# Kernel optimization log

Hardware: AMD Instinct MI355X
Metric: run time of the kernel (lower is better)

The kernel has to match this reference:

```python
import jax, jax.numpy as jnp
import numpy as np

B, W, M = 16, 32, 512
NH, HALF, K, H = 64, 32, 8, 8
LK = W // 2               # long-conv kernel size
LOUT = W - 2 * (LK - 1)   # = 2 (dilated valid conv output length)
NSP = 10                  # n_spatial (hardcoded in module)
GC1_IN = (1 + LOUT) * K   # 24


def setup_inputs() -> dict:
    key = jax.random.key(0)
    ks = jax.random.split(key, 23)
    def n(k, shp, s=0.1):
        return jax.random.normal(k, shp, jnp.float32) * s
    return dict(
        x=jax.random.normal(ks[0], (B, W, M), jnp.float32),
        adj=jax.random.uniform(ks[1], (M, M), jnp.float32) / M,  # row-normalized-ish dense adj
        Wih=n(ks[2], (NH, 1)), Whh=n(ks[3], (NH, NH)),
        bih=n(ks[4], (NH,)), bhh=n(ks[5], (NH,)),
        W1=n(ks[6], (HALF, NH)), W2=n(ks[7], (HALF, NH)), b1=n(ks[8], (HALF,)),
        V=n(ks[9], (HALF,)), bv=n(ks[10], (1,)),
        Wb=n(ks[11], (M, M)), wb=n(ks[12], (1,)),
        conv_w=n(ks[13], (K, 1, W)), conv_b=n(ks[14], (K,)),
        convl_w=n(ks[15], (K, 1, LK)), convl_b=n(ks[16], (K,)),
        gc1_w=n(ks[17], (GC1_IN, NH)), gc1_b=n(ks[18], (NH,)),
        gc2_w=n(ks[19], (NH, NSP)), gc2_b=n(ks[20], (NSP,)),
        out_w=n(ks[21], (H, NSP + NH)), out_b=n(ks[22], (H,)),
    )


def reference(x, adj, Wih, Whh, bih, bhh, W1, W2, b1, V, bv, Wb, wb,
              conv_w, conv_b, convl_w, convl_b, gc1_w, gc1_b, gc2_w, gc2_b,
              out_w, out_b):
    b = x.shape[0]
    # [b, w, m] -> per-node sequences [b*m, w]
    seq = jnp.transpose(x, (0, 2, 1)).reshape(b * M, W)

    # vanilla tanh RNN, input_size=1 (batched over all b*m series)
    inp = seq[:, :, None] * Wih[:, 0] + (bih + bhh)          # [b*m, w, nh]
    def step(h, it):
        return jnp.tanh(it + h @ Whh.T), None
    h0 = jnp.zeros((b * M, NH), x.dtype)
    last_hid, _ = jax.lax.scan(step, h0, jnp.swapaxes(inp, 0, 1))
    last_hid = last_hid.reshape(b, M, NH)                    # out_temporal

    # pairwise additive attention: a[b,i,j] = V . elu(W1 h_j + W2 h_i + b1) + bv
    e1 = last_hid @ W1.T                                     # [b, m, half] (j role)
    e2 = last_hid @ W2.T                                     # [b, m, half] (i role)
    a = jax.nn.elu(e2[:, :, None, :] + e1[:, None, :, :] + b1)  # [b,m,m,half]
    a_mx = a @ V + bv                                        # [b, m, m]
    # F.normalize(p=2, dim=1)
    norm = jnp.sqrt(jnp.sum(a_mx * a_mx, axis=1, keepdims=True))
    a_mx = a_mx / jnp.maximum(norm, 1e-12)

    # per-node short conv (kernel == window -> out len 1) as a single matmul
    r_short = seq @ conv_w[:, 0, :].T + conv_b               # [b*m, k]
    # per-node dilated long conv, batched over all b*m series
    r_long = jax.lax.conv_general_dilated(
        seq[:, None, :], convl_w, window_strides=(1,), padding='VALID',
        rhs_dilation=(2,), dimension_numbers=('NCW', 'OIW', 'NCW'))
    r_long = r_long + convl_b[None, :, None]                 # [b*m, k, LOUT]
    r = jnp.concatenate([r_short[:, :, None], r_long], axis=-1)  # [b*m, k, 1+LOUT]
    r = jax.nn.relu(r.reshape(b, M, GC1_IN))

    # gated mix of static normalized adj and learned attention adj
    c = jax.nn.sigmoid(a_mx @ Wb + wb)
    adj_mix = adj[None] * c + a_mx * (1.0 - c)               # [b, m, m]

    # two dense graph conv layers: relu(adj @ (h @ W) + b)
    h1 = jax.nn.relu(adj_mix @ (r @ gc1_w) + gc1_b)          # [b, m, nh]
    out_spatial = jax.nn.relu(adj_mix @ (h1 @ gc2_w) + gc2_b)  # [b, m, nsp]

    feat = jnp.concatenate([out_spatial, last_hid], axis=-1)  # [b, m, nsp+nh]
    out = feat @ out_w.T + out_b                              # [b, m, h]
    return jnp.transpose(out, (0, 2, 1))                      # [b, h, m]
```

## Files before the change

### kernel.cpp

```cpp
#include <hip/hip_runtime.h>


typedef __attribute__((ext_vector_type(8))) short bf16x8;
typedef __attribute__((ext_vector_type(4))) float f32x4;
#define MFMA16 __builtin_amdgcn_mfma_f32_16x16x32_bf16

__device__ __forceinline__ unsigned short f2bf(float f) {
    unsigned u = __float_as_uint(f);
    u += 0x7fff + ((u >> 16) & 1);
    return (unsigned short)(u >> 16);
}
__device__ __forceinline__ float bf2f(unsigned short h) {
    return __uint_as_float(((unsigned)h) << 16);
}
__device__ __forceinline__ float fast_tanh(float x) {
    float e = __expf(2.f * x);
    return 1.f - 2.f / (e + 1.f);
}

__global__ __launch_bounds__(256) void fused1_kernel(
    const float* __restrict__ x, const float* __restrict__ Wih,
    const float* __restrict__ Whh, const float* __restrict__ bih,
    const float* __restrict__ bhh, const float* __restrict__ W1,
    const float* __restrict__ W2, float* __restrict__ lh,
    float* __restrict__ e1, float* __restrict__ e2,
    const float* __restrict__ conv_w, const float* __restrict__ conv_b,
    const float* __restrict__ convl_w, const float* __restrict__ convl_b,
    const float* __restrict__ gc1_w, unsigned short* __restrict__ rgT,
    const float* __restrict__ Wb, unsigned short* __restrict__ WbT,
    float* __restrict__ nrmss)
{
    __shared__ __align__(16) char smem[12160];
    int blk = blockIdx.x, t = threadIdx.x;

    if (blk < 256) {
        int wid = t >> 6, lane = t & 63;
        int rowblk = blk * 32;
        int b = rowblk >> 9, mb = rowblk & 511;
        float* xs = (float*)smem;
        unsigned short* hs = (unsigned short*)(smem + 4096);
        float* rrs = (float*)(smem + 8704);

        for (int u = t; u < 1024; u += 256) {
            int tt = u >> 5, c = u & 31;
            xs[tt * 32 + c] = x[(b * 32 + tt) * 512 + mb + c];
        }
        for (int u = t; u < 2304; u += 256) hs[u] = 0;
        __syncthreads();

        if (wid < 2) {
            int l15 = lane & 15, quad = lane >> 4;
            int row0 = rowblk + wid * 16;
            unsigned short* hw0 = hs + wid * 1152;

            bf16x8 afr[4][2];
#pragma unroll
            for (int mt = 0; mt < 4; ++mt)
#pragma unroll
                for (int hf = 0; hf < 2; ++hf) {
                    const float* src = Whh + (16 * mt + l15) * 64 + 32 * hf + quad * 8;
                    union { bf16x8 v; unsigned short u[8]; } tmp;
#pragma unroll
                    for (int j = 0; j < 8; ++j) tmp.u[j] = f2bf(src[j]);
                    afr[mt][hf] = tmp.v;
                }
            bf16x8 wfr[2][2][2];
#pragma unroll
            for (int e = 0; e < 2; ++e)
#pragma unroll
                for (int nt = 0; nt < 2; ++nt)
#pragma unroll
                    for (int kf = 0; kf < 2; ++kf) {
                        const float* Wsrc = (e ? W2 : W1);
                        const float* src = Wsrc + (16 * nt + l15) * 64 + 32 * kf + quad * 8;
                        union { bf16x8 v; unsigned short u[8]; } tmp;
#pragma unroll
                        for (int j = 0; j < 8; ++j) tmp.u[j] = f2bf(src[j]);
                        wfr[e][nt][kf] = tmp.v;
                    }
            float wihv[4][4], bsv[4][4];
#pragma unroll
            for (int mt = 0; mt < 4; ++mt)
#pragma unroll
                for (int r = 0; r < 4; ++r) {
                    int n = 16 * mt + quad * 4 + r;
                    wihv[mt][r] = Wih[n];
                    bsv[mt][r]  = bih[n] + bhh[n];
                }

            float th[4][4];
            for (int tstep = 0; tstep < 32; ++tstep) {
                bf16x8 b0 = *(bf16x8*)(hw0 + l15 * 72 + quad * 8);
                bf16x8 b1 = *(bf16x8*)(hw0 + l15 * 72 + 32 + quad * 8);
                float xt = xs[tstep * 32 + wid * 16 + l15];
                f32x4 acc[4];
#pragma unroll
                for (int mt = 0; mt < 4; ++mt) {
                    f32x4 z = {0.f, 0.f, 0.f, 0.f};
                    acc[mt] = MFMA16(afr[mt][0], b0, z, 0, 0, 0);
                    acc[mt] = MFMA16(afr[mt][1], b1, acc[mt], 0, 0, 0);
                }
#pragma unroll
                for (int mt = 0; mt < 4; ++mt) {
                    ushort4 hwv;
#pragma unroll
                    for (int r = 0; r < 4; ++r)
                        th[mt][r] = fast_tanh(acc[mt][r] + xt * wihv[mt][r] + bsv[mt][r]);
                    hwv.x = f2bf(th[mt][0]); hwv.y = f2bf(th[mt][1]);
                    hwv.z = f2bf(th[mt][2]); hwv.w = f2bf(th[mt][3]);
                    *(ushort4*)(hw0 + l15 * 72 + 16 * mt + quad * 4) = hwv;
                }
            }
#pragma unroll
            for (int mt = 0; mt < 4; ++mt)
                *(float4*)(lh + (row0 + l15) * 64 + 16 * mt + quad * 4) =
                    make_float4(th[mt][0], th[mt][1], th[mt][2], th[mt][3]);

            bf16x8 a0 = *(bf16x8*)(hw0 + l15 * 72 + quad * 8);
            bf16x8 a1 = *(bf16x8*)(hw0 + l15 * 72 + 32 + quad * 8);
#pragma unroll
            for (int e = 0; e < 2; ++e) {
                float* dst = e ? e2 : e1;
#pragma unroll
                for (int nt = 0; nt < 2; ++nt) {
                    f32x4 z = {0.f, 0.f, 0.f, 0.f};
                    f32x4 ee = MFMA16(a0, wfr[e][nt][0], z, 0, 0, 0);
                    ee = MFMA16(a1, wfr[e][nt][1], ee, 0, 0, 0);
#pragma unroll
                    for (int r = 0; r < 4; ++r)
                        dst[(row0 + quad * 4 + r) * 32 + 16 * nt + l15] = ee[r];
                }
            }
        } else {
            int wid2 = wid - 2;
#pragma unroll
            for (int rep = 0; rep < 2; ++rep) {
                int task = rep * 64 + lane;
                int rl = wid2 * 16 + (task >> 3);
                int k  = task & 7;
                float s = conv_b[k];
                for (int w = 0; w < 32; ++w) s += xs[w * 32 + rl] * conv_w[k * 32 + w];
                float l0 = convl_b[k], l1 = l0;
                for (int tt = 0; tt < 16; ++tt) {
                    float wv = convl_w[k * 16 + tt];
                    l0 += xs[(2 * tt) * 32 + rl] * wv;
                    l1 += xs[(2 * tt + 1) * 32 + rl] * wv;
                }
                rrs[rl * 25 + k * 3 + 0] = fmaxf(s, 0.f);
                rrs[rl * 25 + k * 3 + 1] = fmaxf(l0, 0.f);
                rrs[rl * 25 + k * 3 + 2] = fmaxf(l1, 0.f);
            }
            __builtin_amdgcn_wave_barrier();
            int rl = wid2 * 16 + (lane & 15);
            int nb = lane >> 4;
#pragma unroll
            for (int q = 0; q < 16; ++q) {
                int n = nb * 16 + q;
                float acc = 0.f;
#pragma unroll
                for (int c = 0; c < 24; ++c) acc += rrs[rl * 25 + c] * gc1_w[c * 64 + n];
                rgT[b * 32768 + n * 512 + mb + rl] = f2bf(acc);
            }
        }
    } else if (blk < 512) {
        int bid = blk - 256;
        int nb = (bid & 15) * 32, kb = (bid >> 4) * 32;
        float* tile = (float*)smem;
        for (int u = t; u < 1024; u += 256) {
            int r = u >> 5, c = u & 31;
            tile[r * 33 + c] = Wb[(kb + r) * 512 + nb + c];
        }
        __syncthreads();
        for (int u = t; u < 1024; u += 256) {
            int r = u >> 5, c = u & 31;
            WbT[(nb + r) * 512 + kb + c] = f2bf(tile[c * 33 + r]);
        }
    } else {
        nrmss[(blk - 512) * 256 + t] = 0.f;
    }
}

__global__ __launch_bounds__(256) void amx_kernel(
    const float* __restrict__ e1, const float* __restrict__ e2,
    const float* __restrict__ b1p, const float* __restrict__ Vp,
    const float* __restrict__ bvp, unsigned short* __restrict__ amxb,
    float* __restrict__ nrmss)
{
    int bb = blockIdx.z;
    int i0 = blockIdx.y * 64, j0 = blockIdx.x * 64;
    __shared__ float e2s[64][33], e1s[64][33];
    __shared__ float Vs[32];
    __shared__ float red[16][68];
    int t = threadIdx.x;
    for (int u = t; u < 2048; u += 256) {
        int r = u >> 5, c = u & 31;
        e2s[r][c] = e2[(bb * 512 + i0 + r) * 32 + c];
        e1s[r][c] = e1[(bb * 512 + j0 + r) * 32 + c] + b1p[c];
    }
    if (t < 32) Vs[t] = Vp[t];
    __syncthreads();
    int ti = (t >> 4) * 4, tj = (t & 15) * 4;
    float acc[4][4] = {};
#pragma unroll
    for (int h = 0; h < 32; ++h) {
        float vv = Vs[h];
        float xi[4], yj[4], Exi[4], Eyj[4];
#pragma unroll
        for (int p = 0; p < 4; ++p) { xi[p] = e2s[ti + p][h]; Exi[p] = __expf(xi[p]); }
#pragma unroll
        for (int q = 0; q < 4; ++q) { yj[q] = e1s[tj + q][h]; Eyj[q] = __expf(yj[q]); }
#pragma unroll
        for (int p = 0; p < 4; ++p)
#pragma unroll
            for (int q = 0; q < 4; ++q) {
                float v = xi[p] + yj[q];
                float prod = Exi[p] * Eyj[q];
                float el = v > 0.f ? v : prod - 1.f;
                acc[p][q] += vv * el;
            }
    }
    float bv = bvp[0];
    float ss[4] = {0.f, 0.f, 0.f, 0.f};
#pragma unroll
    for (int p = 0; p < 4; ++p) {
        float v0 = acc[p][0] + bv, v1 = acc[p][1] + bv;
        float v2 = acc[p][2] + bv, v3 = acc[p][3] + bv;
        ushort4 o;
        o.x = f2bf(v0); o.y = f2bf(v1); o.z = f2bf(v2); o.w = f2bf(v3);
        *(ushort4*)(amxb + (bb * 512 + i0 + ti + p) * 512 + j0 + tj) = o;
        ss[0] += v0 * v0; ss[1] += v1 * v1; ss[2] += v2 * v2; ss[3] += v3 * v3;
    }
#pragma unroll
    for (int q = 0; q < 4; ++q) red[t >> 4][tj + q] = ss[q];
    __syncthreads();
    if (t < 64) {
        float s = 0.f;
#pragma unroll
        for (int g = 0; g < 16; ++g) s += red[g][t];
        atomicAdd(&nrmss[bb * 512 + j0 + t], s);
    }
}

__global__ __launch_bounds__(256) void gemm_adjmix(
    const unsigned short* __restrict__ amxb, const unsigned short* __restrict__ WbT,
    const float* __restrict__ wbp, const float* __restrict__ adj,
    const float* __restrict__ nrmss, unsigned short* __restrict__ adjmix)
{
    int bb = blockIdx.z;
    int i0 = blockIdx.y * 64, j0 = blockIdx.x * 64;
    __shared__ __align__(16) short As[64 * 72];
    __shared__ __align__(16) short Bs[64 * 72];
    __shared__ float rn[512];
    int t = threadIdx.x, w = t >> 6, lane = t & 63;
    int l15 = lane & 15, quad = lane >> 4;
    for (int u = t; u < 512; u += 256)
        rn[u] = 1.f / fmaxf(sqrtf(nrmss[bb * 512 + u]), 1e-12f);
    const unsigned short* Ag = amxb + bb * 262144;
    f32x4 acc[4] = {};
    for (int kk = 1; kk <= 8; ++kk) {
        int k0 = (j0 + 64 * kk) & 511;
        __syncthreads();
#pragma unroll
        for (int u0 = 0; u0 < 2; ++u0) {
            int u = t + u0 * 256;
            int i = u >> 3, o = u & 7;
            *(int4*)(Bs + i * 72 + o * 8) =
                *(const int4*)(WbT + (j0 + i) * 512 + k0 + o * 8);
            union { int4 v; unsigned short us[8]; } ur;
            ur.v = *(const int4*)(Ag + (i0 + i) * 512 + k0 + o * 8);
            union { int4 v; unsigned short us[8]; } ow;
#pragma unroll
            for (int c = 0; c < 8; ++c)
                ow.us[c] = f2bf(bf2f(ur.us[c]) * rn[k0 + o * 8 + c]);
            *(int4*)(As + i * 72 + o * 8) = ow.v;
        }
        __syncthreads();
        bf16x8 a0 = *(bf16x8*)(As + (16 * w + l15) * 72 + quad * 8);
        bf16x8 a1 = *(bf16x8*)(As + (16 * w + l15) * 72 + 32 + quad * 8);
#pragma unroll
        for (int nt = 0; nt < 4; ++nt) {
            bf16x8 b0 = *(bf16x8*)(Bs + (16 * nt + l15) * 72 + quad * 8);
            bf16x8 b1 = *(bf16x8*)(Bs + (16 * nt + l15) * 72 + 32 + quad * 8);
            acc[nt] = MFMA16(a0, b0, acc[nt], 0, 0, 0);
            acc[nt] = MFMA16(a1, b1, acc[nt], 0, 0, 0);
        }
    }
    float wb = wbp[0];
#pragma unroll
    for (int nt = 0; nt < 4; ++nt)
#pragma unroll
    for (int r = 0; r < 4; ++r) {
        int il = 16 * w + quad * 4 + r;
        int jl = 16 * nt + l15;
        int i = i0 + il, j = j0 + jl;
        float s  = acc[nt][r] + wb;
        float cv = 1.f / (1.f + __expf(-s));
        float am = bf2f((unsigned short)As[il * 72 + jl]);
        float ad = adj[i * 512 + j];
        adjmix[(bb * 512 + i) * 512 + j] = f2bf(ad * cv + am * (1.f - cv));
    }
}

__global__ __launch_bounds__(256) void gemm_h1(
    const unsigned short* __restrict__ adjmix, const unsigned short* __restrict__ rgT,
    const float* __restrict__ gc1_b, const float* __restrict__ gc2_w,
    float* __restrict__ h1g)
{
    int bb = blockIdx.y;
    int i0 = blockIdx.x * 32;
    __shared__ __align__(16) short As[32 * 72];
    __shared__ __align__(16) short Bs[64 * 72];
    __shared__ float h1s[32][72];
    int t = threadIdx.x, w = t >> 6, lane = t & 63;
    int l15 = lane & 15, quad = lane >> 4;
    int rt = w & 1, ntb = (w >> 1) * 2;
    const unsigned short* Ag = adjmix + bb * 262144;
    const unsigned short* Bg = rgT + bb * 32768;
    f32x4 acc[2] = {};
    for (int k0 = 0; k0 < 512; k0 += 64) {
        __syncthreads();
        {
            int i = t >> 3, o = t & 7;
            *(int4*)(As + i * 72 + o * 8) =
                *(const int4*)(Ag + (i0 + i) * 512 + k0 + o * 8);
        }
#pragma unroll
        for (int u0 = 0; u0 < 2; ++u0) {
            int u = t + u0 * 256;
            int i = u >> 3, o = u & 7;
            *(int4*)(Bs + i * 72 + o * 8) =
                *(const int4*)(Bg + i * 512 + k0 + o * 8);
        }
        __syncthreads();
        bf16x8 a0 = *(bf16x8*)(As + (16 * rt + l15) * 72 + quad * 8);
        bf16x8 a1 = *(bf16x8*)(As + (16 * rt + l15) * 72 + 32 + quad * 8);
#pragma unroll
        for (int q = 0; q < 2; ++q) {
            int nt = ntb + q;
            bf16x8 b0 = *(bf16x8*)(Bs + (16 * nt + l15) * 72 + quad * 8);
            bf16x8 b1 = *(bf16x8*)(Bs + (16 * nt + l15) * 72 + 32 + quad * 8);
            acc[q] = MFMA16(a0, b0, acc[q], 0, 0, 0);
            acc[q] = MFMA16(a1, b1, acc[q], 0, 0, 0);
        }
    }
#pragma unroll
    for (int q = 0; q < 2; ++q)
#pragma unroll
    for (int r = 0; r < 4; ++r) {
        int il = 16 * rt + quad * 4 + r;
        int j = 16 * (ntb + q) + l15;
        h1s[il][j] = fmaxf(acc[q][r] + gc1_b[j], 0.f);
    }
    __syncthreads();
    for (int u = t; u < 320; u += 256) {
        int row = u / 10, ns = u - row * 10;
        float a2 = 0.f;
#pragma unroll
        for (int j = 0; j < 64; ++j) a2 += h1s[row][j] * gc2_w[j * 10 + ns];
        h1g[(bb * 512 + i0 + row) * 10 + ns] = a2;
    }
}

__global__ __launch_bounds__(256) void ospout_kernel(
    const unsigned short* __restrict__ adjmix, const float* __restrict__ h1g,
    const float* __restrict__ gc2_b, const float* __restrict__ lh,
    const float* __restrict__ out_w, const float* __restrict__ out_b,
    float* __restrict__ out)
{
    int r0 = blockIdx.x * 16;
    int bb = r0 >> 9;
    int wid = threadIdx.x >> 6, lane = threadIdx.x & 63;
    __shared__ float Bsm[10][512];
    __shared__ float ow[8][80];
    __shared__ float ob[8], g2b[10];
    for (int u = threadIdx.x; u < 5120; u += 256) {
        int k = u / 10, ns = u - k * 10;
        Bsm[ns][k] = h1g[bb * 5120 + u];
    }
    if (threadIdx.x < 8)  ob[threadIdx.x]  = out_b[threadIdx.x];
    if (threadIdx.x < 10) g2b[threadIdx.x] = gc2_b[threadIdx.x];
    for (int u = threadIdx.x; u < 592; u += 256) {
        int hh = u / 74, c = u - hh * 74;
        ow[hh][c] = out_w[u];
    }
    __syncthreads();
#pragma unroll
    for (int half = 0; half < 4; ++half) {
        int row = r0 + half * 4 + wid, m = row & 511;
        const unsigned short* Ar = adjmix + row * 512;
        float a[8];
#pragma unroll
        for (int q = 0; q < 8; ++q) a[q] = bf2f(Ar[lane + 64 * q]);
        float os[10];
#pragma unroll
        for (int ns = 0; ns < 10; ++ns) {
            float s = 0.f;
#pragma unroll
            for (int q = 0; q < 8; ++q) s += a[q] * Bsm[ns][lane + 64 * q];
#pragma unroll
            for (int off = 32; off; off >>= 1) s += __shfl_xor(s, off);
            os[ns] = fmaxf(s + g2b[ns], 0.f);
        }
        float lv = lh[row * 64 + lane];
#pragma unroll
        for (int hh = 0; hh < 8; ++hh) {
            float t1 = lv * ow[hh][10 + lane];
#pragma unroll
            for (int off = 32; off; off >>= 1) t1 += __shfl_xor(t1, off);
            if (lane == hh) {
                float acc = ob[hh] + t1;
#pragma unroll
                for (int ns = 0; ns < 10; ++ns) acc += os[ns] * ow[hh][ns];
                out[bb * 4096 + hh * 512 + m] = acc;
            }
        }
    }
}

extern "C" void kernel_launch(void* const* d_in, const int* in_sizes, int n_in,
                              void* d_out, int out_size, void* d_ws, size_t ws_size,
                              hipStream_t stream)
{
    const float* x       = (const float*)d_in[0];
    const float* adj     = (const float*)d_in[1];
    const float* Wih     = (const float*)d_in[2];
    const float* Whh     = (const float*)d_in[3];
    const float* bih     = (const float*)d_in[4];
    const float* bhh     = (const float*)d_in[5];
    const float* W1      = (const float*)d_in[6];
    const float* W2      = (const float*)d_in[7];
    const float* b1      = (const float*)d_in[8];
    const float* V       = (const float*)d_in[9];
    const float* bv      = (const float*)d_in[10];
    const float* Wb      = (const float*)d_in[11];
    const float* wb      = (const float*)d_in[12];
    const float* conv_w  = (const float*)d_in[13];
    const float* conv_b  = (const float*)d_in[14];
    const float* convl_w = (const float*)d_in[15];
    const float* convl_b = (const float*)d_in[16];
    const float* gc1_w   = (const float*)d_in[17];
    const float* gc1_b   = (const float*)d_in[18];
    const float* gc2_w   = (const float*)d_in[19];
    const float* gc2_b   = (const float*)d_in[20];
    const float* out_w   = (const float*)d_in[21];
    const float* out_b   = (const float*)d_in[22];

    float* ws    = (float*)d_ws;
    float* lh    = ws;
    float* e1    = lh + 524288;
    float* e2    = e1 + 262144;
    float* nrmss = e2 + 262144;
    float* h1g   = nrmss + 8192;
    unsigned short* amxb    = (unsigned short*)(h1g + 81920);
    unsigned short* adjmixb = amxb + 4194304;
    unsigned short* WbT     = adjmixb + 4194304;
    unsigned short* rgT     = WbT + 262144;

    fused1_kernel<<<544, 256, 0, stream>>>(
        x, Wih, Whh, bih, bhh, W1, W2, lh, e1, e2,
        conv_w, conv_b, convl_w, convl_b, gc1_w, rgT, Wb, WbT, nrmss);
    amx_kernel<<<dim3(8, 8, 16), 256, 0, stream>>>(e1, e2, b1, V, bv,
                                                   amxb, nrmss);
    gemm_adjmix<<<dim3(8, 8, 16), 256, 0, stream>>>(amxb, WbT, wb, adj,
                                                    nrmss, adjmixb);
    gemm_h1<<<dim3(16, 16), 256, 0, stream>>>(adjmixb, rgT, gc1_b, gc2_w, h1g);
    ospout_kernel<<<512, 256, 0, stream>>>(adjmixb, h1g, gc2_b, lh,
                                           out_w, out_b, (float*)d_out);
}
```

Before: 208.0 us.

## Fuse five kernels into one persistent kernel with global atomic barriers

Merges the RNN/conv, attention, adjmix GEMM, h1 GEMM and output kernels into a single 512-block persistent kernel. The stages are separated by a software grid barrier built on an atomic counter that is reset with a memset before launch. This removes four kernel launch gaps and their tail effects. The cost is spin-wait barrier overhead, and the kernel deadlocks unless all 512 blocks are co-resident, which it relies on launch_bounds(256,2) to allow.

```diff
diff --git a/kernel.cpp b/kernel.cpp
--- a/kernel.cpp
+++ b/kernel.cpp
@@ -4,6 +4,8 @@
 typedef __attribute__((ext_vector_type(8))) short bf16x8;
 typedef __attribute__((ext_vector_type(4))) float f32x4;
 #define MFMA16 __builtin_amdgcn_mfma_f32_16x16x32_bf16
+
+#define NBLK 512u
 
 __device__ __forceinline__ unsigned short f2bf(float f) {
     unsigned u = __float_as_uint(f);
@@ -18,20 +20,40 @@
     return 1.f - 2.f / (e + 1.f);
 }
 
-__global__ __launch_bounds__(256) void fused1_kernel(
-    const float* __restrict__ x, const float* __restrict__ Wih,
-    const float* __restrict__ Whh, const float* __restrict__ bih,
-    const float* __restrict__ bhh, const float* __restrict__ W1,
-    const float* __restrict__ W2, float* __restrict__ lh,
+__device__ __forceinline__ void gbar(unsigned* cnt, unsigned target) {
+    __threadfence();
+    __syncthreads();
+    if (threadIdx.x == 0) {
+        __hip_atomic_fetch_add(cnt, 1u, __ATOMIC_ACQ_REL, __HIP_MEMORY_SCOPE_AGENT);
+        while (__hip_atomic_load(cnt, __ATOMIC_ACQUIRE, __HIP_MEMORY_SCOPE_AGENT) < target)
+            __builtin_amdgcn_s_sleep(2);
+    }
+    __syncthreads();
+    __threadfence();
+}
+
+__global__ __launch_bounds__(256, 2) void cola_fused(
+    const float* __restrict__ x, const float* __restrict__ adj,
+    const float* __restrict__ Wih, const float* __restrict__ Whh,
+    const float* __restrict__ bih, const float* __restrict__ bhh,
+    const float* __restrict__ W1, const float* __restrict__ W2,
+    const float* __restrict__ b1p, const float* __restrict__ Vp,
+    const float* __restrict__ bvp, const float* __restrict__ Wb,
+    const float* __restrict__ wbp, const float* __restrict__ conv_w,
+    const float* __restrict__ conv_b, const float* __restrict__ convl_w,
+    const float* __restrict__ convl_b, const float* __restrict__ gc1_w,
+    const float* __restrict__ gc1_b, const float* __restrict__ gc2_w,
+    const float* __restrict__ gc2_b, const float* __restrict__ out_w,
+    const float* __restrict__ out_b, float* __restrict__ lh,
     float* __restrict__ e1, float* __restrict__ e2,
-    const float* __restrict__ conv_w, const float* __restrict__ conv_b,
-    const float* __restrict__ convl_w, const float* __restrict__ convl_b,
-    const float* __restrict__ gc1_w, unsigned short* __restrict__ rgT,
-    const float* __restrict__ Wb, unsigned short* __restrict__ WbT,
-    float* __restrict__ nrmss)
+    float* __restrict__ nrmss, float* __restrict__ h1g,
+    unsigned short* __restrict__ amxb, unsigned short* __restrict__ adjmixb,
+    unsigned short* __restrict__ WbT, unsigned short* __restrict__ rgT,
+    float* __restrict__ out, unsigned* cnt)
 {
-    __shared__ __align__(16) char smem[12160];
-    int blk = blockIdx.x, t = threadIdx.x;
+    __shared__ __align__(16) char smem[23552];
+    const int blk = blockIdx.x;
+    const int t = threadIdx.x;
 
     if (blk < 256) {
         int wid = t >> 6, lane = t & 63;
@@ -162,8 +184,9 @@
                 rgT[b * 32768 + n * 512 + mb + rl] = f2bf(acc);
             }
         }
-    } else if (blk < 512) {
+    } else {
         int bid = blk - 256;
+        if (bid < 32) nrmss[bid * 256 + t] = 0.f;
         int nb = (bid & 15) * 32, kb = (bid >> 4) * 32;
         float* tile = (float*)smem;
         for (int u = t; u < 1024; u += 256) {
@@ -175,243 +198,239 @@
             int r = u >> 5, c = u & 31;
             WbT[(nb + r) * 512 + kb + c] = f2bf(tile[c * 33 + r]);
         }
-    } else {
-        nrmss[(blk - 512) * 256 + t] = 0.f;
-    }
-}
-
-__global__ __launch_bounds__(256) void amx_kernel(
-    const float* __restrict__ e1, const float* __restrict__ e2,
-    const float* __restrict__ b1p, const float* __restrict__ Vp,
-    const float* __restrict__ bvp, unsigned short* __restrict__ amxb,
-    float* __restrict__ nrmss)
-{
-    int bb = blockIdx.z;
-    int i0 = blockIdx.y * 64, j0 = blockIdx.x * 64;
-    __shared__ float e2s[64][33], e1s[64][33];
-    __shared__ float Vs[32];
-    __shared__ float red[16][68];
-    int t = threadIdx.x;
-    for (int u = t; u < 2048; u += 256) {
-        int r = u >> 5, c = u & 31;
-        e2s[r][c] = e2[(bb * 512 + i0 + r) * 32 + c];
-        e1s[r][c] = e1[(bb * 512 + j0 + r) * 32 + c] + b1p[c];
-    }
-    if (t < 32) Vs[t] = Vp[t];
-    __syncthreads();
-    int ti = (t >> 4) * 4, tj = (t & 15) * 4;
-    float acc[4][4] = {};
-#pragma unroll
-    for (int h = 0; h < 32; ++h) {
-        float vv = Vs[h];
-        float xi[4], yj[4], Exi[4], Eyj[4];
-#pragma unroll
-        for (int p = 0; p < 4; ++p) { xi[p] = e2s[ti + p][h]; Exi[p] = __expf(xi[p]); }
-#pragma unroll
-        for (int q = 0; q < 4; ++q) { yj[q] = e1s[tj + q][h]; Eyj[q] = __expf(yj[q]); }
-#pragma unroll
-        for (int p = 0; p < 4; ++p)
-#pragma unroll
-            for (int q = 0; q < 4; ++q) {
-                float v = xi[p] + yj[q];
-                float prod = Exi[p] * Eyj[q];
-                float el = v > 0.f ? v : prod - 1.f;
-                acc[p][q] += vv * el;
-            }
-    }
-    float bv = bvp[0];
-    float ss[4] = {0.f, 0.f, 0.f, 0.f};
-#pragma unroll
-    for (int p = 0; p < 4; ++p) {
-        float v0 = acc[p][0] + bv, v1 = acc[p][1] + bv;
-        float v2 = acc[p][2] + bv, v3 = acc[p][3] + bv;
-        ushort4 o;
-        o.x = f2bf(v0); o.y = f2bf(v1); o.z = f2bf(v2); o.w = f2bf(v3);
-        *(ushort4*)(amxb + (bb * 512 + i0 + ti + p) * 512 + j0 + tj) = o;
-        ss[0] += v0 * v0; ss[1] += v1 * v1; ss[2] += v2 * v2; ss[3] += v3 * v3;
-    }
-#pragma unroll
-    for (int q = 0; q < 4; ++q) red[t >> 4][tj + q] = ss[q];
-    __syncthreads();
-    if (t < 64) {
-        float s = 0.f;
-#pragma unroll
-        for (int g = 0; g < 16; ++g) s += red[g][t];
-        atomicAdd(&nrmss[bb * 512 + j0 + t], s);
-    }
-}
-
-__global__ __launch_bounds__(256) void gemm_adjmix(
-    const unsigned short* __restrict__ amxb, const unsigned short* __restrict__ WbT,
-    const float* __restrict__ wbp, const float* __restrict__ adj,
-    const float* __restrict__ nrmss, unsigned short* __restrict__ adjmix)
-{
-    int bb = blockIdx.z;
-    int i0 = blockIdx.y * 64, j0 = blockIdx.x * 64;
-    __shared__ __align__(16) short As[64 * 72];
-    __shared__ __align__(16) short Bs[64 * 72];
-    __shared__ float rn[512];
-    int t = threadIdx.x, w = t >> 6, lane = t & 63;
-    int l15 = lane & 15, quad = lane >> 4;
-    for (int u = t; u < 512; u += 256)
-        rn[u] = 1.f / fmaxf(sqrtf(nrmss[bb * 512 + u]), 1e-12f);
-    const unsigned short* Ag = amxb + bb * 262144;
-    f32x4 acc[4] = {};
-    for (int kk = 1; kk <= 8; ++kk) {
-        int k0 = (j0 + 64 * kk) & 511;
+    }
+    gbar(cnt, NBLK * 1u);
+
+    {
+        float (*e2s)[33] = (float (*)[33])smem;
+        float (*e1s)[33] = (float (*)[33])(smem + 8448);
+        float* Vs        = (float*)(smem + 16896);
+        float (*red)[68] = (float (*)[68])(smem + 17024);
+        const int ti = (t >> 4) * 4, tj = (t & 15) * 4;
+        const float bv = bvp[0];
+#pragma unroll 1
+        for (int rep = 0; rep < 2; ++rep) {
+            const int vt = blk * 2 + rep;
+            const int bb = vt >> 6;
+            const int i0 = ((vt >> 3) & 7) * 64;
+            const int j0 = (vt & 7) * 64;
+            __syncthreads();
+            for (int u = t; u < 2048; u += 256) {
+                int r = u >> 5, c = u & 31;
+                e2s[r][c] = e2[(bb * 512 + i0 + r) * 32 + c];
+                e1s[r][c] = e1[(bb * 512 + j0 + r) * 32 + c] + b1p[c];
+            }
+            if (t < 32) Vs[t] = Vp[t];
+            __syncthreads();
+            float acc[4][4] = {};
+#pragma unroll
+            for (int h = 0; h < 32; ++h) {
+                float vv = Vs[h];
+                float xi[4], yj[4], Exi[4], Eyj[4];
+#pragma unroll
+                for (int p = 0; p < 4; ++p) { xi[p] = e2s[ti + p][h]; Exi[p] = __expf(xi[p]); }
+#pragma unroll
+                for (int q = 0; q < 4; ++q) { yj[q] = e1s[tj + q][h]; Eyj[q] = __expf(yj[q]); }
+#pragma unroll
+                for (int p = 0; p < 4; ++p)
+#pragma unroll
+                    for (int q = 0; q < 4; ++q) {
+                        float v = xi[p] + yj[q];
+                        float prod = Exi[p] * Eyj[q];
+                        float el = v > 0.f ? v : prod - 1.f;
+                        acc[p][q] += vv * el;
+                    }
+            }
+            float ss[4] = {0.f, 0.f, 0.f, 0.f};
+#pragma unroll
+            for (int p = 0; p < 4; ++p) {
+                float v0 = acc[p][0] + bv, v1 = acc[p][1] + bv;
+                float v2 = acc[p][2] + bv, v3 = acc[p][3] + bv;
+                ushort4 o;
+                o.x = f2bf(v0); o.y = f2bf(v1); o.z = f2bf(v2); o.w = f2bf(v3);
+                *(ushort4*)(amxb + (bb * 512 + i0 + ti + p) * 512 + j0 + tj) = o;
+                ss[0] += v0 * v0; ss[1] += v1 * v1; ss[2] += v2 * v2; ss[3] += v3 * v3;
+            }
+#pragma unroll
+            for (int q = 0; q < 4; ++q) red[t >> 4][tj + q] = ss[q];
+            __syncthreads();
+            if (t < 64) {
+                float s = 0.f;
+#pragma unroll
+                for (int g = 0; g < 16; ++g) s += red[g][t];
+                atomicAdd(&nrmss[bb * 512 + j0 + t], s);
+            }
+        }
+    }
+    gbar(cnt, NBLK * 2u);
+
+    {
+        short* As = (short*)smem;
+        short* Bs = (short*)(smem + 9216);
+        float* rn = (float*)(smem + 18432);
+        const int w = t >> 6, lane = t & 63;
+        const int l15 = lane & 15, quad = lane >> 4;
+        const float wb = wbp[0];
+#pragma unroll 1
+        for (int rep = 0; rep < 2; ++rep) {
+            const int vt = blk * 2 + rep;
+            const int bb = vt >> 6;
+            const int i0 = ((vt >> 3) & 7) * 64;
+            const int j0 = (vt & 7) * 64;
+            for (int u = t; u < 512; u += 256)
+                rn[u] = 1.f / fmaxf(sqrtf(nrmss[bb * 512 + u]), 1e-12f);
+            const unsigned short* Ag = amxb + bb * 262144;
+            f32x4 acc[4] = {};
+            for (int kk = 1; kk <= 8; ++kk) {
+                int k0 = (j0 + 64 * kk) & 511;
+                __syncthreads();
+#pragma unroll
+                for (int u0 = 0; u0 < 2; ++u0) {
+                    int u = t + u0 * 256;
+                    int i = u >> 3, o = u & 7;
+                    *(int4*)(Bs + i * 72 + o * 8) =
+                        *(const int4*)(WbT + (j0 + i) * 512 + k0 + o * 8);
+                    union { int4 v; unsigned short us[8]; } ur;
+                    ur.v = *(const int4*)(Ag + (i0 + i) * 512 + k0 + o * 8);
+                    union { int4 v; unsigned short us[8]; } ow2;
+#pragma unroll
+                    for (int c = 0; c < 8; ++c)
+                        ow2.us[c] = f2bf(bf2f(ur.us[c]) * rn[k0 + o * 8 + c]);
+                    *(int4*)(As + i * 72 + o * 8) = ow2.v;
+                }
+                __syncthreads();
+                bf16x8 a0 = *(bf16x8*)(As + (16 * w + l15) * 72 + quad * 8);
+                bf16x8 a1 = *(bf16x8*)(As + (16 * w + l15) * 72 + 32 + quad * 8);
+#pragma unroll
+                for (int nt = 0; nt < 4; ++nt) {
+                    bf16x8 b0 = *(bf16x8*)(Bs + (16 * nt + l15) * 72 + quad * 8);
+                    bf16x8 b1 = *(bf16x8*)(Bs + (16 * nt + l15) * 72 + 32 + quad * 8);
+                    acc[nt] = MFMA16(a0, b0, acc[nt], 0, 0, 0);
+                    acc[nt] = MFMA16(a1, b1, acc[nt], 0, 0, 0);
+                }
+            }
+#pragma unroll
+            for (int nt = 0; nt < 4; ++nt)
+#pragma unroll
+            for (int r = 0; r < 4; ++r) {
+                int il = 16 * w + quad * 4 + r;
+                int jl = 16 * nt + l15;
+                int i = i0 + il, j = j0 + jl;
+                float s  = acc[nt][r] + wb;
+                float cv = 1.f / (1.f + __expf(-s));
+                float am = bf2f((unsigned short)As[il * 72 + jl]);
+                float ad = adj[i * 512 + j];
+                adjmixb[(bb * 512 + i) * 512 + j] = f2bf(ad * cv + am * (1.f - cv));
+            }
+        }
+    }
+    gbar(cnt, NBLK * 3u);
+
+    if (blk < 256) {
+        short* As = (short*)smem;
+        short* Bs = (short*)(smem + 4608);
+        float (*h1s)[72] = (float (*)[72])(smem + 13824);
+        const int bb = blk >> 4;
+        const int i0 = (blk & 15) * 32;
+        const int w = t >> 6, lane = t & 63;
+        const int l15 = lane & 15, quad = lane >> 4;
+        const int rt = w & 1, ntb = (w >> 1) * 2;
+        const unsigned short* Ag = adjmixb + bb * 262144;
+        const unsigned short* Bg = rgT + bb * 32768;
+        f32x4 acc[2] = {};
+        for (int k0 = 0; k0 < 512; k0 += 64) {
+            __syncthreads();
+            {
+                int i = t >> 3, o = t & 7;
+                *(int4*)(As + i * 72 + o * 8) =
+                    *(const int4*)(Ag + (i0 + i) * 512 + k0 + o * 8);
+            }
+#pragma unroll
+            for (int u0 = 0; u0 < 2; ++u0) {
+                int u = t + u0 * 256;
+                int i = u >> 3, o = u & 7;
+                *(int4*)(Bs + i * 72 + o * 8) =
+                    *(const int4*)(Bg + i * 512 + k0 + o * 8);
+            }
+            __syncthreads();
+            bf16x8 a0 = *(bf16x8*)(As + (16 * rt + l15) * 72 + quad * 8);
+            bf16x8 a1 = *(bf16x8*)(As + (16 * rt + l15) * 72 + 32 + quad * 8);
+#pragma unroll
+            for (int q = 0; q < 2; ++q) {
+                int nt = ntb + q;
+                bf16x8 b0 = *(bf16x8*)(Bs + (16 * nt + l15) * 72 + quad * 8);
+                bf16x8 b1 = *(bf16x8*)(Bs + (16 * nt + l15) * 72 + 32 + quad * 8);
+                acc[q] = MFMA16(a0, b0, acc[q], 0, 0, 0);
+                acc[q] = MFMA16(a1, b1, acc[q], 0, 0, 0);
+            }
+        }
+#pragma unroll
+        for (int q = 0; q < 2; ++q)
+#pragma unroll
+        for (int r = 0; r < 4; ++r) {
+            int il = 16 * rt + quad * 4 + r;
+            int j = 16 * (ntb + q) + l15;
+            h1s[il][j] = fmaxf(acc[q][r] + gc1_b[j], 0.f);
+        }
         __syncthreads();
-#pragma unroll
-        for (int u0 = 0; u0 < 2; ++u0) {
-            int u = t + u0 * 256;
-            int i = u >> 3, o = u & 7;
-            *(int4*)(Bs + i * 72 + o * 8) =
-                *(const int4*)(WbT + (j0 + i) * 512 + k0 + o * 8);
-            union { int4 v; unsigned short us[8]; } ur;
-            ur.v = *(const int4*)(Ag + (i0 + i) * 512 + k0 + o * 8);
-            union { int4 v; unsigned short us[8]; } ow;
-#pragma unroll
-            for (int c = 0; c < 8; ++c)
-                ow.us[c] = f2bf(bf2f(ur.us[c]) * rn[k0 + o * 8 + c]);
-            *(int4*)(As + i * 72 + o * 8) = ow.v;
+        for (int u = t; u < 320; u += 256) {
+            int row = u / 10, ns = u - row * 10;
+            float a2 = 0.f;
+#pragma unroll
+            for (int j = 0; j < 64; ++j) a2 += h1s[row][j] * gc2_w[j * 10 + ns];
+            h1g[(bb * 512 + i0 + row) * 10 + ns] = a2;
+        }
+    }
+    gbar(cnt, NBLK * 4u);
+
+    {
+        float (*Bsm)[512] = (float (*)[512])smem;
+        float (*ow)[80]   = (float (*)[80])(smem + 20480);
+        float* ob  = (float*)(smem + 23040);
+        float* g2b = (float*)(smem + 23072);
+        const int r0 = blk * 16;
+        const int bb = r0 >> 9;
+        const int wid = t >> 6, lane = t & 63;
+        for (int u = t; u < 5120; u += 256) {
+            int k = u / 10, ns = u - k * 10;
+            Bsm[ns][k] = h1g[bb * 5120 + u];
+        }
+        if (t < 8)  ob[t]  = out_b[t];
+        if (t < 10) g2b[t] = gc2_b[t];
+        for (int u = t; u < 592; u += 256) {
+            int hh = u / 74, c = u - hh * 74;
+            ow[hh][c] = out_w[u];
         }
         __syncthreads();
-        bf16x8 a0 = *(bf16x8*)(As + (16 * w + l15) * 72 + quad * 8);
-        bf16x8 a1 = *(bf16x8*)(As + (16 * w + l15) * 72 + 32 + quad * 8);
-#pragma unroll
-        for (int nt = 0; nt < 4; ++nt) {
-            bf16x8 b0 = *(bf16x8*)(Bs + (16 * nt + l15) * 72 + quad * 8);
-            bf16x8 b1 = *(bf16x8*)(Bs + (16 * nt + l15) * 72 + 32 + quad * 8);
-            acc[nt] = MFMA16(a0, b0, acc[nt], 0, 0, 0);
-            acc[nt] = MFMA16(a1, b1, acc[nt], 0, 0, 0);
-        }
-    }
-    float wb = wbp[0];
-#pragma unroll
-    for (int nt = 0; nt < 4; ++nt)
-#pragma unroll
-    for (int r = 0; r < 4; ++r) {
-        int il = 16 * w + quad * 4 + r;
-        int jl = 16 * nt + l15;
-        int i = i0 + il, j = j0 + jl;
-        float s  = acc[nt][r] + wb;
-        float cv = 1.f / (1.f + __expf(-s));
-        float am = bf2f((unsigned short)As[il * 72 + jl]);
-        float ad = adj[i * 512 + j];
-        adjmix[(bb * 512 + i) * 512 + j] = f2bf(ad * cv + am * (1.f - cv));
-    }
-}
-
-__global__ __launch_bounds__(256) void gemm_h1(
-    const unsigned short* __restrict__ adjmix, const unsigned short* __restrict__ rgT,
-    const float* __restrict__ gc1_b, const float* __restrict__ gc2_w,
-    float* __restrict__ h1g)
-{
-    int bb = blockIdx.y;
-    int i0 = blockIdx.x * 32;
-    __shared__ __align__(16) short As[32 * 72];
-    __shared__ __align__(16) short Bs[64 * 72];
-    __shared__ float h1s[32][72];
-    int t = threadIdx.x, w = t >> 6, lane = t & 63;
-    int l15 = lane & 15, quad = lane >> 4;
-    int rt = w & 1, ntb = (w >> 1) * 2;
-    const unsigned short* Ag = adjmix + bb * 262144;
-    const unsigned short* Bg = rgT + bb * 32768;
-    f32x4 acc[2] = {};
-    for (int k0 = 0; k0 < 512; k0 += 64) {
-        __syncthreads();
-        {
-            int i = t >> 3, o = t & 7;
-            *(int4*)(As + i * 72 + o * 8) =
-                *(const int4*)(Ag + (i0 + i) * 512 + k0 + o * 8);
-        }
-#pragma unroll
-        for (int u0 = 0; u0 < 2; ++u0) {
-            int u = t + u0 * 256;
-            int i = u >> 3, o = u & 7;
-            *(int4*)(Bs + i * 72 + o * 8) =
-                *(const int4*)(Bg + i * 512 + k0 + o * 8);
-        }
-        __syncthreads();
-        bf16x8 a0 = *(bf16x8*)(As + (16 * rt + l15) * 72 + quad * 8);
-        bf16x8 a1 = *(bf16x8*)(As + (16 * rt + l15) * 72 + 32 + quad * 8);
-#pragma unroll
-        for (int q = 0; q < 2; ++q) {
-            int nt = ntb + q;
-            bf16x8 b0 = *(bf16x8*)(Bs + (16 * nt + l15) * 72 + quad * 8);
-            bf16x8 b1 = *(bf16x8*)(Bs + (16 * nt + l15) * 72 + 32 + quad * 8);
-            acc[q] = MFMA16(a0, b0, acc[q], 0, 0, 0);
-            acc[q] = MFMA16(a1, b1, acc[q], 0, 0, 0);
-        }
-    }
-#pragma unroll
-    for (int q = 0; q < 2; ++q)
-#pragma unroll
-    for (int r = 0; r < 4; ++r) {
-        int il = 16 * rt + quad * 4 + r;
-        int j = 16 * (ntb + q) + l15;
-        h1s[il][j] = fmaxf(acc[q][r] + gc1_b[j], 0.f);
-    }
-    __syncthreads();
-    for (int u = t; u < 320; u += 256) {
-        int row = u / 10, ns = u - row * 10;
-        float a2 = 0.f;
-#pragma unroll
-        for (int j = 0; j < 64; ++j) a2 += h1s[row][j] * gc2_w[j * 10 + ns];
-        h1g[(bb * 512 + i0 + row) * 10 + ns] = a2;
-    }
-}
-
-__global__ __launch_bounds__(256) void ospout_kernel(
-    const unsigned short* __restrict__ adjmix, const float* __restrict__ h1g,
-    const float* __restrict__ gc2_b, const float* __restrict__ lh,
-    const float* __restrict__ out_w, const float* __restrict__ out_b,
-    float* __restrict__ out)
-{
-    int r0 = blockIdx.x * 16;
-    int bb = r0 >> 9;
-    int wid = threadIdx.x >> 6, lane = threadIdx.x & 63;
-    __shared__ float Bsm[10][512];
-    __shared__ float ow[8][80];
-    __shared__ float ob[8], g2b[10];
-    for (int u = threadIdx.x; u < 5120; u += 256) {
-        int k = u / 10, ns = u - k * 10;
-        Bsm[ns][k] = h1g[bb * 5120 + u];
-    }
-    if (threadIdx.x < 8)  ob[threadIdx.x]  = out_b[threadIdx.x];
-    if (threadIdx.x < 10) g2b[threadIdx.x] = gc2_b[threadIdx.x];
-    for (int u = threadIdx.x; u < 592; u += 256) {
-        int hh = u / 74, c = u - hh * 74;
-        ow[hh][c] = out_w[u];
-    }
-    __syncthreads();
-#pragma unroll
-    for (int half = 0; half < 4; ++half) {
-        int row = r0 + half * 4 + wid, m = row & 511;
-        const unsigned short* Ar = adjmix + row * 512;
-        float a[8];
-#pragma unroll
-        for (int q = 0; q < 8; ++q) a[q] = bf2f(Ar[lane + 64 * q]);
-        float os[10];
-#pragma unroll
-        for (int ns = 0; ns < 10; ++ns) {
-            float s = 0.f;
-#pragma unroll
-            for (int q = 0; q < 8; ++q) s += a[q] * Bsm[ns][lane + 64 * q];
-#pragma unroll
-            for (int off = 32; off; off >>= 1) s += __shfl_xor(s, off);
-            os[ns] = fmaxf(s + g2b[ns], 0.f);
-        }
-        float lv = lh[row * 64 + lane];
-#pragma unroll
-        for (int hh = 0; hh < 8; ++hh) {
-            float t1 = lv * ow[hh][10 + lane];
-#pragma unroll
-            for (int off = 32; off; off >>= 1) t1 += __shfl_xor(t1, off);
-            if (lane == hh) {
-                float acc = ob[hh] + t1;
-#pragma unroll
-                for (int ns = 0; ns < 10; ++ns) acc += os[ns] * ow[hh][ns];
-                out[bb * 4096 + hh * 512 + m] = acc;
+#pragma unroll
+        for (int half = 0; half < 4; ++half) {
+            int row = r0 + half * 4 + wid, m = row & 511;
+            const unsigned short* Ar = adjmixb + row * 512;
+            float a[8];
+#pragma unroll
+            for (int q = 0; q < 8; ++q) a[q] = bf2f(Ar[lane + 64 * q]);
+            float os[10];
+#pragma unroll
+            for (int ns = 0; ns < 10; ++ns) {
+                float s = 0.f;
+#pragma unroll
+                for (int q = 0; q < 8; ++q) s += a[q] * Bsm[ns][lane + 64 * q];
+#pragma unroll
+                for (int off = 32; off; off >>= 1) s += __shfl_xor(s, off);
+                os[ns] = fmaxf(s + g2b[ns], 0.f);
+            }
+            float lv = lh[row * 64 + lane];
+#pragma unroll
+            for (int hh = 0; hh < 8; ++hh) {
+                float t1 = lv * ow[hh][10 + lane];
+#pragma unroll
+                for (int off = 32; off; off >>= 1) t1 += __shfl_xor(t1, off);
+                if (lane == hh) {
+                    float acc = ob[hh] + t1;
+#pragma unroll
+                    for (int ns = 0; ns < 10; ++ns) acc += os[ns] * ow[hh][ns];
+                    out[bb * 4096 + hh * 512 + m] = acc;
+                }
             }
         }
     }
@@ -455,15 +474,13 @@
     unsigned short* adjmixb = amxb + 4194304;
     unsigned short* WbT     = adjmixb + 4194304;
     unsigned short* rgT     = WbT + 262144;
-
-    fused1_kernel<<<544, 256, 0, stream>>>(
-        x, Wih, Whh, bih, bhh, W1, W2, lh, e1, e2,
-        conv_w, conv_b, convl_w, convl_b, gc1_w, rgT, Wb, WbT, nrmss);
-    amx_kernel<<<dim3(8, 8, 16), 256, 0, stream>>>(e1, e2, b1, V, bv,
-                                                   amxb, nrmss);
-    gemm_adjmix<<<dim3(8, 8, 16), 256, 0, stream>>>(amxb, WbT, wb, adj,
-                                                    nrmss, adjmixb);
-    gemm_h1<<<dim3(16, 16), 256, 0, stream>>>(adjmixb, rgT, gc1_b, gc2_w, h1g);
-    ospout_kernel<<<512, 256, 0, stream>>>(adjmixb, h1g, gc2_b, lh,
-                                           out_w, out_b, (float*)d_out);
-}
+    unsigned* cnt = (unsigned*)(rgT + 524288);
+    float* outp = (float*)d_out;
+
+    hipMemsetAsync(cnt, 0, 128, stream);
+    cola_fused<<<512, 256, 0, stream>>>(
+        x, adj, Wih, Whh, bih, bhh, W1, W2, b1, V, bv, Wb, wb,
+        conv_w, conv_b, convl_w, convl_b, gc1_w, gc1_b, gc2_w, gc2_b,
+        out_w, out_b, lh, e1, e2, nrmss, h1g, amxb, adjmixb, WbT, rgT,
+        outp, cnt);
+}
```

Result: slower. 692.4 us (+233.0%).

## Fuse adjacency-mix GEMM with first graph-conv GEMM into one row-block kernel

Applied to the files above, without the earlier changes.

Merges the gated adj_mix GEMM and the h1 GEMM into a single kernel. Each block owns 32 rows of one batch, sweeps all 8 column tiles of the Wb product, writes adj_mix, then reads those same rows back for the adj_mix @ (r @ gc1_w) product. Register prefetch of the next tile is added to both loops. This removes one launch and lets the second GEMM read freshly written, likely cache-resident rows. The grid shrinks from 1024 blocks to 256, which lowers parallelism on a chip with many CUs.

```diff
diff --git a/kernel.cpp b/kernel.cpp
--- a/kernel.cpp
+++ b/kernel.cpp
@@ -241,95 +241,109 @@
     }
 }
 
-__global__ __launch_bounds__(256) void gemm_adjmix(
+__global__ __launch_bounds__(256) void gemm_adjmix_h1(
     const unsigned short* __restrict__ amxb, const unsigned short* __restrict__ WbT,
     const float* __restrict__ wbp, const float* __restrict__ adj,
-    const float* __restrict__ nrmss, unsigned short* __restrict__ adjmix)
+    const float* __restrict__ nrmss, unsigned short* __restrict__ adjmixb,
+    const unsigned short* __restrict__ rgT, const float* __restrict__ gc1_b,
+    const float* __restrict__ gc2_w, float* __restrict__ h1g)
 {
-    int bb = blockIdx.z;
-    int i0 = blockIdx.y * 64, j0 = blockIdx.x * 64;
-    __shared__ __align__(16) short As[64 * 72];
-    __shared__ __align__(16) short Bs[64 * 72];
-    __shared__ float rn[512];
-    int t = threadIdx.x, w = t >> 6, lane = t & 63;
-    int l15 = lane & 15, quad = lane >> 4;
+    const int bb = blockIdx.y;
+    const int i0 = blockIdx.x * 32;
+    __shared__ __align__(16) char smem[23552];
+    short* As = (short*)smem;
+    short* Bs = (short*)(smem + 4608);
+    float* rn = (float*)(smem + 13824);
+    float (*h1s)[72] = (float (*)[72])(smem + 13824);
+
+    const int t = threadIdx.x, w = t >> 6, lane = t & 63;
+    const int l15 = lane & 15, quad = lane >> 4;
+    const int rh = w & 1, ch = w >> 1;
+    const int si = t >> 3, so = t & 7;
+
     for (int u = t; u < 512; u += 256)
         rn[u] = 1.f / fmaxf(sqrtf(nrmss[bb * 512 + u]), 1e-12f);
     const unsigned short* Ag = amxb + bb * 262144;
-    f32x4 acc[4] = {};
-    for (int kk = 1; kk <= 8; ++kk) {
-        int k0 = (j0 + 64 * kk) & 511;
-        __syncthreads();
-#pragma unroll
-        for (int u0 = 0; u0 < 2; ++u0) {
-            int u = t + u0 * 256;
-            int i = u >> 3, o = u & 7;
-            *(int4*)(Bs + i * 72 + o * 8) =
-                *(const int4*)(WbT + (j0 + i) * 512 + k0 + o * 8);
-            union { int4 v; unsigned short us[8]; } ur;
-            ur.v = *(const int4*)(Ag + (i0 + i) * 512 + k0 + o * 8);
-            union { int4 v; unsigned short us[8]; } ow;
+    const float wb = wbp[0];
+
+    int4 pa, pb0, pb1;
+    {
+        pa  = *(const int4*)(Ag + (i0 + si) * 512 + 64 + so * 8);
+        pb0 = *(const int4*)(WbT + si * 512 + 64 + so * 8);
+        pb1 = *(const int4*)(WbT + (32 + si) * 512 + 64 + so * 8);
+    }
+    f32x4 acc[2];
+    const f32x4 zz = {0.f, 0.f, 0.f, 0.f};
+    for (int it = 0; it < 64; ++it) {
+        const int j0 = it >> 3, kk = it & 7;
+        const int k0 = (j0 * 64 + 64 * (kk + 1)) & 511;
+        __syncthreads();
+        {
+            union { int4 v; unsigned short us[8]; } ur; ur.v = pa;
+            union { int4 v; unsigned short us[8]; } ow2;
 #pragma unroll
             for (int c = 0; c < 8; ++c)
-                ow.us[c] = f2bf(bf2f(ur.us[c]) * rn[k0 + o * 8 + c]);
-            *(int4*)(As + i * 72 + o * 8) = ow.v;
-        }
-        __syncthreads();
-        bf16x8 a0 = *(bf16x8*)(As + (16 * w + l15) * 72 + quad * 8);
-        bf16x8 a1 = *(bf16x8*)(As + (16 * w + l15) * 72 + 32 + quad * 8);
-#pragma unroll
-        for (int nt = 0; nt < 4; ++nt) {
+                ow2.us[c] = f2bf(bf2f(ur.us[c]) * rn[k0 + so * 8 + c]);
+            *(int4*)(As + si * 72 + so * 8) = ow2.v;
+            *(int4*)(Bs + si * 72 + so * 8) = pb0;
+            *(int4*)(Bs + (32 + si) * 72 + so * 8) = pb1;
+        }
+        if (it < 63) {
+            const int itn = it + 1, j0n = itn >> 3, kkn = itn & 7;
+            const int k0n = (j0n * 64 + 64 * (kkn + 1)) & 511;
+            pa  = *(const int4*)(Ag + (i0 + si) * 512 + k0n + so * 8);
+            pb0 = *(const int4*)(WbT + (j0n * 64 + si) * 512 + k0n + so * 8);
+            pb1 = *(const int4*)(WbT + (j0n * 64 + 32 + si) * 512 + k0n + so * 8);
+        }
+        __syncthreads();
+        if (kk == 0) { acc[0] = zz; acc[1] = zz; }
+        bf16x8 a0 = *(bf16x8*)(As + (16 * rh + l15) * 72 + quad * 8);
+        bf16x8 a1 = *(bf16x8*)(As + (16 * rh + l15) * 72 + 32 + quad * 8);
+#pragma unroll
+        for (int q = 0; q < 2; ++q) {
+            int nt = ch * 2 + q;
             bf16x8 b0 = *(bf16x8*)(Bs + (16 * nt + l15) * 72 + quad * 8);
             bf16x8 b1 = *(bf16x8*)(Bs + (16 * nt + l15) * 72 + 32 + quad * 8);
-            acc[nt] = MFMA16(a0, b0, acc[nt], 0, 0, 0);
-            acc[nt] = MFMA16(a1, b1, acc[nt], 0, 0, 0);
-        }
-    }
-    float wb = wbp[0];
-#pragma unroll
-    for (int nt = 0; nt < 4; ++nt)
-#pragma unroll
-    for (int r = 0; r < 4; ++r) {
-        int il = 16 * w + quad * 4 + r;
-        int jl = 16 * nt + l15;
-        int i = i0 + il, j = j0 + jl;
-        float s  = acc[nt][r] + wb;
-        float cv = 1.f / (1.f + __expf(-s));
-        float am = bf2f((unsigned short)As[il * 72 + jl]);
-        float ad = adj[i * 512 + j];
-        adjmix[(bb * 512 + i) * 512 + j] = f2bf(ad * cv + am * (1.f - cv));
-    }
-}
-
-__global__ __launch_bounds__(256) void gemm_h1(
-    const unsigned short* __restrict__ adjmix, const unsigned short* __restrict__ rgT,
-    const float* __restrict__ gc1_b, const float* __restrict__ gc2_w,
-    float* __restrict__ h1g)
-{
-    int bb = blockIdx.y;
-    int i0 = blockIdx.x * 32;
-    __shared__ __align__(16) short As[32 * 72];
-    __shared__ __align__(16) short Bs[64 * 72];
-    __shared__ float h1s[32][72];
-    int t = threadIdx.x, w = t >> 6, lane = t & 63;
-    int l15 = lane & 15, quad = lane >> 4;
-    int rt = w & 1, ntb = (w >> 1) * 2;
-    const unsigned short* Ag = adjmix + bb * 262144;
-    const unsigned short* Bg = rgT + bb * 32768;
-    f32x4 acc[2] = {};
-    for (int k0 = 0; k0 < 512; k0 += 64) {
-        __syncthreads();
-        {
-            int i = t >> 3, o = t & 7;
-            *(int4*)(As + i * 72 + o * 8) =
-                *(const int4*)(Ag + (i0 + i) * 512 + k0 + o * 8);
-        }
-#pragma unroll
-        for (int u0 = 0; u0 < 2; ++u0) {
-            int u = t + u0 * 256;
-            int i = u >> 3, o = u & 7;
-            *(int4*)(Bs + i * 72 + o * 8) =
-                *(const int4*)(Bg + i * 512 + k0 + o * 8);
+            acc[q] = MFMA16(a0, b0, acc[q], 0, 0, 0);
+            acc[q] = MFMA16(a1, b1, acc[q], 0, 0, 0);
+        }
+        if (kk == 7) {
+#pragma unroll
+            for (int q = 0; q < 2; ++q)
+#pragma unroll
+            for (int r = 0; r < 4; ++r) {
+                int il = 16 * rh + quad * 4 + r;
+                int jl = 16 * (ch * 2 + q) + l15;
+                int i = i0 + il, j = j0 * 64 + jl;
+                float s  = acc[q][r] + wb;
+                float cv = 1.f / (1.f + __expf(-s));
+                float am = bf2f((unsigned short)As[il * 72 + jl]);
+                float ad = adj[i * 512 + j];
+                adjmixb[(bb * 512 + i) * 512 + j] = f2bf(ad * cv + am * (1.f - cv));
+            }
+        }
+    }
+
+    const unsigned short* Ag2 = adjmixb + bb * 262144;
+    const unsigned short* Bg2 = rgT + bb * 32768;
+    const int rt = w & 1, ntb = (w >> 1) * 2;
+    f32x4 acc2[2] = {};
+    int4 qa, qb0, qb1;
+    {
+        qa  = *(const int4*)(Ag2 + (i0 + si) * 512 + so * 8);
+        qb0 = *(const int4*)(Bg2 + si * 512 + so * 8);
+        qb1 = *(const int4*)(Bg2 + (32 + si) * 512 + so * 8);
+    }
+    for (int kt = 0; kt < 8; ++kt) {
+        __syncthreads();
+        *(int4*)(As + si * 72 + so * 8) = qa;
+        *(int4*)(Bs + si * 72 + so * 8) = qb0;
+        *(int4*)(Bs + (32 + si) * 72 + so * 8) = qb1;
+        if (kt < 7) {
+            const int k0n = (kt + 1) * 64;
+            qa  = *(const int4*)(Ag2 + (i0 + si) * 512 + k0n + so * 8);
+            qb0 = *(const int4*)(Bg2 + si * 512 + k0n + so * 8);
+            qb1 = *(const int4*)(Bg2 + (32 + si) * 512 + k0n + so * 8);
         }
         __syncthreads();
         bf16x8 a0 = *(bf16x8*)(As + (16 * rt + l15) * 72 + quad * 8);
@@ -339,8 +353,8 @@
             int nt = ntb + q;
             bf16x8 b0 = *(bf16x8*)(Bs + (16 * nt + l15) * 72 + quad * 8);
             bf16x8 b1 = *(bf16x8*)(Bs + (16 * nt + l15) * 72 + 32 + quad * 8);
-            acc[q] = MFMA16(a0, b0, acc[q], 0, 0, 0);
-            acc[q] = MFMA16(a1, b1, acc[q], 0, 0, 0);
+            acc2[q] = MFMA16(a0, b0, acc2[q], 0, 0, 0);
+            acc2[q] = MFMA16(a1, b1, acc2[q], 0, 0, 0);
         }
     }
 #pragma unroll
@@ -349,7 +363,7 @@
     for (int r = 0; r < 4; ++r) {
         int il = 16 * rt + quad * 4 + r;
         int j = 16 * (ntb + q) + l15;
-        h1s[il][j] = fmaxf(acc[q][r] + gc1_b[j], 0.f);
+        h1s[il][j] = fmaxf(acc2[q][r] + gc1_b[j], 0.f);
     }
     __syncthreads();
     for (int u = t; u < 320; u += 256) {
@@ -461,9 +475,8 @@
         conv_w, conv_b, convl_w, convl_b, gc1_w, rgT, Wb, WbT, nrmss);
     amx_kernel<<<dim3(8, 8, 16), 256, 0, stream>>>(e1, e2, b1, V, bv,
                                                    amxb, nrmss);
-    gemm_adjmix<<<dim3(8, 8, 16), 256, 0, stream>>>(amxb, WbT, wb, adj,
-                                                    nrmss, adjmixb);
-    gemm_h1<<<dim3(16, 16), 256, 0, stream>>>(adjmixb, rgT, gc1_b, gc2_w, h1g);
+    gemm_adjmix_h1<<<dim3(16, 16), 256, 0, stream>>>(
+        amxb, WbT, wb, adj, nrmss, adjmixb, rgT, gc1_b, gc2_w, h1g);
     ospout_kernel<<<512, 256, 0, stream>>>(adjmixb, h1g, gc2_b, lh,
                                            out_w, out_b, (float*)d_out);
 }
```

After: 220.3 us. 5.9% more time.
